# Performance work log

Hardware: AMD Instinct MI355X
Metric: run time of the kernel (lower is better)

## Reference

```python
import jax, jax.numpy as jnp
import numpy as np

IB = 8; WB = 8; ABMVM = 8; ABNM = 8; N_MSB = 4; NL = 0.0  # noise_level=0 -> deterministic
B = 4096; IN = 1024; H = 1024

sg = jax.lax.stop_gradient

def quant_raw(x, bits, r):
    step = 2.0 ** (bits - 1)
    xs = jnp.clip(x / r, -1.0 + 1.0 / step, 1.0 - 1.0 / step)
    return jnp.round(xs * step) / step * r

def quant_ste(x, bits, r):
    # straight-through: value = quantized, grad = identity wrt x, no grad to r
    return x + sg(quant_raw(x, bits, r) - x)

def pact(x, a):
    # sign(x)*0.5*(|x| - ||x|-a| + a) == clamp(x, -a, a), kept literal for fidelity
    return jnp.sign(x) * 0.5 * (jnp.abs(x) - jnp.abs(jnp.abs(x) - a) + a)

def bitsplit(x, bits, n_msb):
    # symmetric bit-splitting; STE backward: each y_i has identity grad wrt x
    ste = x - sg(x)
    xv = sg(x)
    beta = 1.0
    ys = []
    for _ in range(n_msb):
        y = quant_raw(xv / beta, bits, 1.0)
        xv = xv - y * beta
        ys.append(y + ste)
        beta = beta / 2.0
    betas = jnp.asarray([1.0 / (2.0 ** i) for i in range(n_msb)], dtype=x.dtype)
    return jnp.stack(ys), betas  # [n_msb, B, D], [n_msb]

def custom_mm(inp, w, b, key):
    # forward: inp @ (quant(clamp(w)) + noise) + quant(b) + noise
    # backward (torch custom): grads use RAW w/b -> STE via out_lin path
    kw, kb = jax.random.split(key)
    n = inp.shape[0]
    noise_w = jax.random.normal(kw, (n, w.shape[1], w.shape[2]), dtype=w.dtype) * NL
    noise_b = jax.random.normal(kb, (n, 1, b.shape[2]), dtype=b.dtype) * NL
    wq = quant_raw(jnp.clip(w, -1.0, 1.0), WB, 1.0)
    bq = quant_raw(b, WB, 1.0)
    out_val = jnp.einsum('nbi,nio->nbo', inp, wq + noise_w) + (bq + noise_b)
    out_lin = jnp.einsum('nbi,io->nbo', inp, w[0]) + b
    return out_lin + sg(out_val - out_lin)

def _cell(input, hx, cx, weight_ih, weight_hh, bias_ih, bias_hh,
          a1, a3, a4, a5, a6, a7, a8, a9, a10, a11):
    k1, k2 = jax.random.split(jax.random.key(42))
    ys, betas = bitsplit(pact(input, a1) / a1, IB, N_MSB)
    out_q = quant_ste(custom_mm(ys, weight_ih, bias_ih, k1), ABMVM, 1.0)
    part1 = (betas[:, None, None] * out_q).sum(0) * a1          # [B, 4H]
    ys, betas = bitsplit(pact(hx, a11) / a11, IB, N_MSB)
    out_q = quant_ste(custom_mm(ys, weight_hh, bias_hh, k2), ABMVM, 1.0)
    part2 = (betas[:, None, None] * out_q).sum(0) * a11
    gates = part1 + part2
    i, j, f, o = jnp.split(gates, 4, axis=1)
    fg = quant_ste(pact(jax.nn.sigmoid(f), a3), ABNM, a3)
    ig = quant_ste(pact(jax.nn.sigmoid(i), a4), ABNM, a4)
    act = quant_ste(pact(jnp.tanh(j), a5), ABNM, a5)
    og = quant_ste(pact(jax.nn.sigmoid(o), a6), ABNM, a6)
    gc = quant_ste(pact(cx * fg, a7), ABNM, a7)
    ai = quant_ste(pact(ig * act, a8), ABNM, a8)
    new_c = quant_ste(pact(gc + ai, a9), ABNM, a9)
    ac = quant_ste(pact(jnp.tanh(new_c), a10), ABNM, a10)
    new_h = quant_ste(pact(ac * og, a11), ABNM, a11)
    return jnp.stack([new_h, new_c])  # [2, B, H]

def setup_inputs() -> dict:
    key = jax.random.key(0)
    ks = jax.random.split(key, 7)
    return {
        'input': jax.random.normal(ks[0], (B, IN), dtype=jnp.float32),
        'hx': jax.random.normal(ks[1], (B, H), dtype=jnp.float32),
        'cx': jax.random.normal(ks[2], (B, H), dtype=jnp.float32),
        'weight_ih': jax.random.normal(ks[3], (1, IN, 4 * H), dtype=jnp.float32) * 0.05,
        'weight_hh': jax.random.normal(ks[4], (1, H, 4 * H), dtype=jnp.float32) * 0.05,
        'bias_ih': jax.random.normal(ks[5], (1, 1, 4 * H), dtype=jnp.float32) * 0.05,
        'bias_hh': jax.random.normal(ks[6], (1, 1, 4 * H), dtype=jnp.float32) * 0.05,
        'a1': jnp.array([128.0]), 'a3': jnp.array([1.0]), 'a4': jnp.array([1.0]),
        'a5': jnp.array([1.0]), 'a6': jnp.array([1.0]), 'a7': jnp.array([4.0]),
        'a8': jnp.array([1.0]), 'a9': jnp.array([4.0]), 'a10': jnp.array([1.0]),
        'a11': jnp.array([4.0]),
    }

def reference(input, hx, cx, weight_ih, weight_hh, bias_ih, bias_hh,
              a1, a3, a4, a5, a6, a7, a8, a9, a10, a11):
    return _cell(input, hx, cx, weight_ih, weight_hh, bias_ih, bias_hh,
                 a1, a3, a4, a5, a6, a7, a8, a9, a10, a11)
```

## Files before the change

### kernel.cpp

```cpp
#include <hip/hip_runtime.h>
#include <cstdint>

typedef unsigned short u16;
typedef __attribute__((ext_vector_type(4))) int i32x4;

#define DEVI __device__ __forceinline__

DEVI float pactf(float x, float a) {
    float ax = fabsf(x);
    float w  = fabsf(ax - a);
    float t  = (ax - w) + a;
    float s  = (x > 0.f) ? 0.5f : ((x < 0.f) ? -0.5f : 0.0f);
    return s * t;
}
DEVI float quantf(float x, float r) {
    float xs = x / r;
    xs = fminf(fmaxf(xs, -0.9921875f), 0.9921875f);
    float e = rintf(xs * 128.0f);
    return (e * 0.0078125f) * r;
}
DEVI float sigf(float x) {
    float eg  = (float)exp(-(double)x);
    float den = 1.0f + eg;
    return 1.0f / den;
}
DEVI float tanf32(float x) { return (float)tanh((double)x); }

#define KSIG  4436
#define NSIG  8873
#define KTANH 2309
#define NTANH 4619

__global__ void prep_tables(float* __restrict__ Ts, float* __restrict__ Tt) {
    int i = blockIdx.x * 256 + threadIdx.x;
    if (i < NSIG)  Ts[i] = sigf((float)(i - KSIG)  * 0.00390625f);
    if (i < NTANH) Tt[i] = tanf32((float)(i - KTANH) * 0.00390625f);
}

DEVI float sig_lut(float g, const float* __restrict__ Ts) {
    float g256 = g * 256.0f;
    float kf = rintf(g256);
    if (kf == g256) {
        if (kf >  (float)KSIG) return 1.0f;
        if (kf < -(float)KSIG) return 0.0f;
        return Ts[(int)kf + KSIG];
    }
    return sigf(g);
}
DEVI float tanh_lut(float g, const float* __restrict__ Tt) {
    float g256 = g * 256.0f;
    float kf = rintf(g256);
    if (kf == g256) {
        if (fabsf(kf) <= (float)KTANH) return Tt[(int)kf + KTANH];
        return copysignf(1.0f, g);
    }
    return tanf32(g);
}

__global__ void prep_act_f(const float* __restrict__ X, const float* __restrict__ ap,
                           signed char* __restrict__ A, int planebase) {
    int idx4 = (blockIdx.x * 256 + threadIdx.x) * 4;
    float a = ap[0];
    float4 xv4 = *(const float4*)(X + idx4);
    float v[4] = {xv4.x, xv4.y, xv4.z, xv4.w};
    signed char e4[4][4];
#pragma unroll
    for (int el = 0; el < 4; el++) {
        float x = pactf(v[el], a) / a;
        float xv = x;
        float beta = 1.0f;
#pragma unroll
        for (int n = 0; n < 4; n++) {
            float xs = xv / beta;
            xs = fminf(fmaxf(xs, -0.9921875f), 0.9921875f);
            float e = rintf(xs * 128.0f);
            e4[n][el] = (signed char)(int)e;
            float y = e * 0.0078125f;
            xv = xv - y * beta;
            beta = beta * 0.5f;
        }
    }
#pragma unroll
    for (int n = 0; n < 4; n++)
        *(char4*)(A + (size_t)(planebase + n) * 4194304u + idx4) =
            make_char4(e4[n][0], e4[n][1], e4[n][2], e4[n][3]);
}

__global__ void prep_w(const float* __restrict__ W0, const float* __restrict__ W1,
                       signed char* __restrict__ Wt) {
    __shared__ float tile[32][33];
    int proj = blockIdx.z;
    const float* W = proj ? W1 : W0;
    int n0 = blockIdx.x * 32, k0 = blockIdx.y * 32;
    int tx = threadIdx.x, ty = threadIdx.y;
#pragma unroll
    for (int i = 0; i < 4; i++)
        tile[ty + i * 8][tx] = W[(size_t)(k0 + ty + i * 8) * 4096 + n0 + tx];
    __syncthreads();
#pragma unroll
    for (int i = 0; i < 4; i++) {
        float w = tile[tx][ty + i * 8];
        float xs = fminf(fmaxf(w, -0.9921875f), 0.9921875f);
        float e = rintf(xs * 128.f);
        Wt[(size_t)proj * 4194304u + (size_t)(n0 + ty + i * 8) * 1024 + k0 + tx] =
            (signed char)(int)e;
    }
}

__global__ void prep_bias(const float* __restrict__ b0, const float* __restrict__ b1,
                          float* __restrict__ Bf) {
    int idx = blockIdx.x * 256 + threadIdx.x;
    const float* b = (idx < 4096) ? b0 : b1;
    float v = b[idx & 4095];
    float xs = fminf(fmaxf(v, -0.9921875f), 0.9921875f);
    Bf[idx] = rintf(xs * 128.f);
}

#define GLOAD16(gp, lp) __builtin_amdgcn_global_load_lds( \
    (const __attribute__((address_space(1))) void*)(gp),  \
    (__attribute__((address_space(3))) void*)(lp), 16, 0, 0)

__global__ __launch_bounds__(256) void gemm_planes(
    const signed char* __restrict__ A, const signed char* __restrict__ Wt,
    const float* __restrict__ Bf, signed char* __restrict__ E) {
    __shared__ __align__(16) signed char lds[16384];
    int tid = threadIdx.x;
    int c0 = blockIdx.x * 128;
    int r0 = blockIdx.y * 128;
    int proj = (r0 >= 16384) ? 1 : 0;

    const signed char* gA = A + (size_t)(r0 + (tid >> 2)) * 1024 + (tid & 3) * 16;
    const signed char* gB = Wt + (size_t)proj * 4194304u + (size_t)(c0 + (tid >> 2)) * 1024 + (tid & 3) * 16;

    signed char* lA0 = lds + tid * 16;
    signed char* lA1 = lds + 4096 + tid * 16;
    signed char* lB0 = lds + 8192 + tid * 16;
    signed char* lB1 = lds + 12288 + tid * 16;

    int w = tid >> 6, l = tid & 63;
    int wm = (w >> 1) * 64, wn = (w & 1) * 64;
    int quad = l >> 4, lrow = l & 15;

    const signed char* fA = lds + (wm + lrow) * 64 + quad * 16;
    const signed char* fB = lds + 8192 + (wn + lrow) * 64 + quad * 16;

    i32x4 acc[4][4] = {};

    for (int k0 = 0; k0 < 1024; k0 += 64) {
        GLOAD16(gA, lA0);
        GLOAD16(gA + 64 * 1024, lA1);
        GLOAD16(gB, lB0);
        GLOAD16(gB + 64 * 1024, lB1);
        gA += 64; gB += 64;
        asm volatile("s_waitcnt vmcnt(0)" ::: "memory");
        __syncthreads();
        i32x4 af[4], bfr[4];
#pragma unroll
        for (int mt = 0; mt < 4; mt++) af[mt] = *(const i32x4*)(fA + mt * 1024);
#pragma unroll
        for (int nt = 0; nt < 4; nt++) bfr[nt] = *(const i32x4*)(fB + nt * 1024);
#pragma unroll
        for (int mt = 0; mt < 4; mt++)
#pragma unroll
            for (int nt = 0; nt < 4; nt++)
                acc[mt][nt] = __builtin_amdgcn_mfma_i32_16x16x64_i8(
                    af[mt], bfr[nt], acc[mt][nt], 0, 0, 0);
        __syncthreads();
    }

    signed char* ctile = lds;
#pragma unroll
    for (int nt = 0; nt < 4; nt++) {
        int lc = wn + nt * 16 + lrow;
        float bb = Bf[proj * 4096 + c0 + lc];
#pragma unroll
        for (int mt = 0; mt < 4; mt++) {
            int lr = wm + mt * 16 + quad * 4;
#pragma unroll
            for (int r = 0; r < 4; r++) {
                float t = (float)acc[mt][nt][r] * 0.0078125f + bb;
                float tc = fminf(fmaxf(t, -127.f), 127.f);
                ctile[(lr + r) * 128 + lc] = (signed char)(int)rintf(tc);
            }
        }
    }
    __syncthreads();
#pragma unroll
    for (int p = 0; p < 4; p++) {
        int lr = (tid >> 3) + p * 32;
        int lc = (tid & 7) * 16;
        *(int4*)(E + (size_t)(r0 + lr) * 4096 + c0 + lc) =
            *(const int4*)(ctile + lr * 128 + lc);
    }
}

__global__ __launch_bounds__(256) void gates_kernel_t(
    const signed char* __restrict__ E, const float* __restrict__ cx,
    float* __restrict__ out,
    const float* __restrict__ TsG, const float* __restrict__ TtG,
    const float* __restrict__ a1p, const float* __restrict__ a3p,
    const float* __restrict__ a4p, const float* __restrict__ a5p,
    const float* __restrict__ a6p, const float* __restrict__ a7p,
    const float* __restrict__ a8p, const float* __restrict__ a9p,
    const float* __restrict__ a10p, const float* __restrict__ a11p) {
    __shared__ float Ts[NSIG];
    __shared__ float Tt[NTANH];
    int tid = threadIdx.x;
    for (int i = tid; i < NSIG; i += 256) Ts[i] = TsG[i];
    for (int i = tid; i < NTANH; i += 256) Tt[i] = TtG[i];
    __syncthreads();

    int b = blockIdx.x;
    int h0 = tid * 4;
    float a1 = a1p[0], a3 = a3p[0], a4 = a4p[0], a5 = a5p[0], a6 = a6p[0];
    float a7 = a7p[0], a8 = a8p[0], a9 = a9p[0], a10 = a10p[0], a11 = a11p[0];

    float gate[4][4];
#pragma unroll
    for (int g = 0; g < 4; g++) {
        size_t colbase = (size_t)g * 1024 + h0;
        int s1[4] = {0, 0, 0, 0}, s2[4] = {0, 0, 0, 0};
#pragma unroll
        for (int n = 0; n < 4; n++) {
            char4 e1 = *(const char4*)(E + (((size_t)(n * 4096 + b)) << 12) + colbase);
            char4 e2 = *(const char4*)(E + (((size_t)((4 + n) * 4096 + b)) << 12) + colbase);
            int wgt = 8 >> n;
            s1[0] += (int)e1.x * wgt; s1[1] += (int)e1.y * wgt;
            s1[2] += (int)e1.z * wgt; s1[3] += (int)e1.w * wgt;
            s2[0] += (int)e2.x * wgt; s2[1] += (int)e2.y * wgt;
            s2[2] += (int)e2.z * wgt; s2[3] += (int)e2.w * wgt;
        }
#pragma unroll
        for (int jj = 0; jj < 4; jj++) {
            float p1 = ((float)s1[jj] * 0.0009765625f) * a1;
            float p2 = ((float)s2[jj] * 0.0009765625f) * a11;
            gate[g][jj] = p1 + p2;
        }
    }

    float4 cxv = *(const float4*)(cx + (size_t)b * 1024 + h0);
    float cxa[4] = {cxv.x, cxv.y, cxv.z, cxv.w};
    float nh[4], ncv[4];
#pragma unroll
    for (int jj = 0; jj < 4; jj++) {
        float gi = gate[0][jj], gj = gate[1][jj], gf = gate[2][jj], go = gate[3][jj];
        float fg  = quantf(pactf(sig_lut(gf, Ts), a3), a3);
        float ig  = quantf(pactf(sig_lut(gi, Ts), a4), a4);
        float act = quantf(pactf(tanh_lut(gj, Tt), a5), a5);
        float og  = quantf(pactf(sig_lut(go, Ts), a6), a6);
        float gc  = quantf(pactf(cxa[jj] * fg, a7), a7);
        float ai  = quantf(pactf(ig * act, a8), a8);
        float nc  = quantf(pactf(gc + ai, a9), a9);
        float ac  = quantf(pactf(tanh_lut(nc, Tt), a10), a10);
        float hh  = quantf(pactf(ac * og, a11), a11);
        nh[jj]  = hh;
        ncv[jj] = nc;
    }
    float4 o1 = {nh[0], nh[1], nh[2], nh[3]};
    float4 o2 = {ncv[0], ncv[1], ncv[2], ncv[3]};
    *(float4*)(out + (size_t)b * 1024 + h0) = o1;
    *(float4*)(out + 4194304u + (size_t)b * 1024 + h0) = o2;
}

extern "C" void kernel_launch(void* const* d_in, const int* in_sizes, int n_in,
                              void* d_out, int out_size, void* d_ws, size_t ws_size,
                              hipStream_t stream) {
    const float* input = (const float*)d_in[0];
    const float* hx    = (const float*)d_in[1];
    const float* cx    = (const float*)d_in[2];
    const float* wih   = (const float*)d_in[3];
    const float* whh   = (const float*)d_in[4];
    const float* bih   = (const float*)d_in[5];
    const float* bhh   = (const float*)d_in[6];
    const float* a1  = (const float*)d_in[7];
    const float* a3  = (const float*)d_in[8];
    const float* a4  = (const float*)d_in[9];
    const float* a5  = (const float*)d_in[10];
    const float* a6  = (const float*)d_in[11];
    const float* a7  = (const float*)d_in[12];
    const float* a8  = (const float*)d_in[13];
    const float* a9  = (const float*)d_in[14];
    const float* a10 = (const float*)d_in[15];
    const float* a11 = (const float*)d_in[16];

    char* ws = (char*)d_ws;
    signed char* A  = (signed char*)ws;
    signed char* Wt = (signed char*)(ws + 33554432);
    float*       Bf = (float*)(ws + 41943040);
    float*       Ts = (float*)(ws + 41975808);
    float*       Tt = (float*)(ws + 42011300);
    signed char* E  = (signed char*)(ws + 42041344);

    prep_tables<<<35, 256, 0, stream>>>(Ts, Tt);
    prep_act_f<<<4096, 256, 0, stream>>>(input, a1, A, 0);
    prep_act_f<<<4096, 256, 0, stream>>>(hx, a11, A, 4);
    prep_w<<<dim3(128, 32, 2), dim3(32, 8), 0, stream>>>(wih, whh, Wt);
    prep_bias<<<32, 256, 0, stream>>>(bih, bhh, Bf);
    gemm_planes<<<dim3(32, 256), 256, 0, stream>>>(A, Wt, Bf, E);
    gates_kernel_t<<<4096, 256, 0, stream>>>(E, cx, (float*)d_out, Ts, Tt,
                                             a1, a3, a4, a5, a6, a7, a8, a9, a10, a11);
}
```

Before: 380.1 us.

## Double-buffer GEMM LDS tiles, merge prep kernels, read LUTs from global

The int8 plane GEMM now uses two LDS buffers, so the next K-slice is loaded by global_load_lds while MFMAs run on the current one. This removes the per-iteration full vmcnt(0) stall, at the cost of doubling LDS per block, which may lower occupancy. The table and bias prep kernels are merged, and the two activation-prep launches become one, cutting launch count. The gates kernel stops copying the sigmoid/tanh tables into shared memory and reads them from global memory, which avoids about 54KB of LDS fill per block but makes the lookups go through the cache.

```diff
diff --git a/kernel.cpp b/kernel.cpp
--- a/kernel.cpp
+++ b/kernel.cpp
@@ -30,12 +30,6 @@
 #define NSIG  8873
 #define KTANH 2309
 #define NTANH 4619
-
-__global__ void prep_tables(float* __restrict__ Ts, float* __restrict__ Tt) {
-    int i = blockIdx.x * 256 + threadIdx.x;
-    if (i < NSIG)  Ts[i] = sigf((float)(i - KSIG)  * 0.00390625f);
-    if (i < NTANH) Tt[i] = tanf32((float)(i - KTANH) * 0.00390625f);
-}
 
 DEVI float sig_lut(float g, const float* __restrict__ Ts) {
     float g256 = g * 256.0f;
@@ -57,10 +51,29 @@
     return tanf32(g);
 }
 
-__global__ void prep_act_f(const float* __restrict__ X, const float* __restrict__ ap,
-                           signed char* __restrict__ A, int planebase) {
-    int idx4 = (blockIdx.x * 256 + threadIdx.x) * 4;
-    float a = ap[0];
+__global__ void prep_misc(const float* __restrict__ b0, const float* __restrict__ b1,
+                          float* __restrict__ Bf, float* __restrict__ Ts,
+                          float* __restrict__ Tt) {
+    int i = blockIdx.x * 256 + threadIdx.x;
+    if (i < NSIG)  Ts[i] = sigf((float)(i - KSIG)  * 0.00390625f);
+    if (i < NTANH) Tt[i] = tanf32((float)(i - KTANH) * 0.00390625f);
+    if (i < 8192) {
+        const float* b = (i < 4096) ? b0 : b1;
+        float v = b[i & 4095];
+        float xs = fminf(fmaxf(v, -0.9921875f), 0.9921875f);
+        Bf[i] = rintf(xs * 128.f);
+    }
+}
+
+__global__ void prep_act2(const float* __restrict__ X0, const float* __restrict__ X1,
+                          const float* __restrict__ a1p, const float* __restrict__ a11p,
+                          signed char* __restrict__ A) {
+    int blk = blockIdx.x;
+    int lo = (blk < 4096) ? 1 : 0;
+    const float* X = lo ? X0 : X1;
+    float a = lo ? a1p[0] : a11p[0];
+    int planebase = lo ? 0 : 4;
+    int idx4 = ((blk & 4095) * 256 + threadIdx.x) * 4;
     float4 xv4 = *(const float4*)(X + idx4);
     float v[4] = {xv4.x, xv4.y, xv4.z, xv4.w};
     signed char e4[4][4];
@@ -107,15 +120,6 @@
     }
 }
 
-__global__ void prep_bias(const float* __restrict__ b0, const float* __restrict__ b1,
-                          float* __restrict__ Bf) {
-    int idx = blockIdx.x * 256 + threadIdx.x;
-    const float* b = (idx < 4096) ? b0 : b1;
-    float v = b[idx & 4095];
-    float xs = fminf(fmaxf(v, -0.9921875f), 0.9921875f);
-    Bf[idx] = rintf(xs * 128.f);
-}
-
 #define GLOAD16(gp, lp) __builtin_amdgcn_global_load_lds( \
     (const __attribute__((address_space(1))) void*)(gp),  \
     (__attribute__((address_space(3))) void*)(lp), 16, 0, 0)
@@ -123,7 +127,7 @@
 __global__ __launch_bounds__(256) void gemm_planes(
     const signed char* __restrict__ A, const signed char* __restrict__ Wt,
     const float* __restrict__ Bf, signed char* __restrict__ E) {
-    __shared__ __align__(16) signed char lds[16384];
+    __shared__ __align__(16) signed char lds[32768];
     int tid = threadIdx.x;
     int c0 = blockIdx.x * 128;
     int r0 = blockIdx.y * 128;
@@ -132,41 +136,57 @@
     const signed char* gA = A + (size_t)(r0 + (tid >> 2)) * 1024 + (tid & 3) * 16;
     const signed char* gB = Wt + (size_t)proj * 4194304u + (size_t)(c0 + (tid >> 2)) * 1024 + (tid & 3) * 16;
 
-    signed char* lA0 = lds + tid * 16;
-    signed char* lA1 = lds + 4096 + tid * 16;
-    signed char* lB0 = lds + 8192 + tid * 16;
-    signed char* lB1 = lds + 12288 + tid * 16;
-
     int w = tid >> 6, l = tid & 63;
     int wm = (w >> 1) * 64, wn = (w & 1) * 64;
     int quad = l >> 4, lrow = l & 15;
 
-    const signed char* fA = lds + (wm + lrow) * 64 + quad * 16;
-    const signed char* fB = lds + 8192 + (wn + lrow) * 64 + quad * 16;
+    int stoff = tid * 16;
+    int fAoff = (wm + lrow) * 64 + quad * 16;
+    int fBoff = 8192 + (wn + lrow) * 64 + quad * 16;
 
     i32x4 acc[4][4] = {};
 
-    for (int k0 = 0; k0 < 1024; k0 += 64) {
-        GLOAD16(gA, lA0);
-        GLOAD16(gA + 64 * 1024, lA1);
-        GLOAD16(gB, lB0);
-        GLOAD16(gB + 64 * 1024, lB1);
-        gA += 64; gB += 64;
-        asm volatile("s_waitcnt vmcnt(0)" ::: "memory");
+#define STAGE(bufbase)                                        \
+    do {                                                      \
+        signed char* lb = lds + (bufbase) + stoff;            \
+        GLOAD16(gA,             lb);                          \
+        GLOAD16(gA + 64 * 1024, lb + 4096);                   \
+        GLOAD16(gB,             lb + 8192);                   \
+        GLOAD16(gB + 64 * 1024, lb + 12288);                  \
+        gA += 64; gB += 64;                                   \
+    } while (0)
+
+#define COMPUTE(bufbase)                                      \
+    do {                                                      \
+        const signed char* fA = lds + (bufbase) + fAoff;      \
+        const signed char* fB = lds + (bufbase) + fBoff;      \
+        i32x4 af[4], bfr[4];                                  \
+        _Pragma("unroll")                                     \
+        for (int mt = 0; mt < 4; mt++) af[mt] = *(const i32x4*)(fA + mt * 1024);  \
+        _Pragma("unroll")                                     \
+        for (int nt = 0; nt < 4; nt++) bfr[nt] = *(const i32x4*)(fB + nt * 1024); \
+        _Pragma("unroll")                                     \
+        for (int mt = 0; mt < 4; mt++)                        \
+            _Pragma("unroll")                                 \
+            for (int nt = 0; nt < 4; nt++)                    \
+                acc[mt][nt] = __builtin_amdgcn_mfma_i32_16x16x64_i8( \
+                    af[mt], bfr[nt], acc[mt][nt], 0, 0, 0);   \
+    } while (0)
+
+    STAGE(0);
+    asm volatile("s_waitcnt vmcnt(0)" ::: "memory");
+    __syncthreads();
+
+    for (int k0 = 0; k0 < 1024; k0 += 128) {
+        STAGE(16384);
+        COMPUTE(0);
         __syncthreads();
-        i32x4 af[4], bfr[4];
-#pragma unroll
-        for (int mt = 0; mt < 4; mt++) af[mt] = *(const i32x4*)(fA + mt * 1024);
-#pragma unroll
-        for (int nt = 0; nt < 4; nt++) bfr[nt] = *(const i32x4*)(fB + nt * 1024);
-#pragma unroll
-        for (int mt = 0; mt < 4; mt++)
-#pragma unroll
-            for (int nt = 0; nt < 4; nt++)
-                acc[mt][nt] = __builtin_amdgcn_mfma_i32_16x16x64_i8(
-                    af[mt], bfr[nt], acc[mt][nt], 0, 0, 0);
+        if (k0 + 128 < 1024) STAGE(0);
+        COMPUTE(16384);
         __syncthreads();
     }
+#undef STAGE
+#undef COMPUTE
 
     signed char* ctile = lds;
 #pragma unroll
@@ -197,19 +217,13 @@
 __global__ __launch_bounds__(256) void gates_kernel_t(
     const signed char* __restrict__ E, const float* __restrict__ cx,
     float* __restrict__ out,
-    const float* __restrict__ TsG, const float* __restrict__ TtG,
+    const float* __restrict__ Ts, const float* __restrict__ Tt,
     const float* __restrict__ a1p, const float* __restrict__ a3p,
     const float* __restrict__ a4p, const float* __restrict__ a5p,
     const float* __restrict__ a6p, const float* __restrict__ a7p,
     const float* __restrict__ a8p, const float* __restrict__ a9p,
     const float* __restrict__ a10p, const float* __restrict__ a11p) {
-    __shared__ float Ts[NSIG];
-    __shared__ float Tt[NTANH];
     int tid = threadIdx.x;
-    for (int i = tid; i < NSIG; i += 256) Ts[i] = TsG[i];
-    for (int i = tid; i < NTANH; i += 256) Tt[i] = TtG[i];
-    __syncthreads();
-
     int b = blockIdx.x;
     int h0 = tid * 4;
     float a1 = a1p[0], a3 = a3p[0], a4 = a4p[0], a5 = a5p[0], a6 = a6p[0];
@@ -291,11 +305,9 @@
     float*       Tt = (float*)(ws + 42011300);
     signed char* E  = (signed char*)(ws + 42041344);
 
-    prep_tables<<<35, 256, 0, stream>>>(Ts, Tt);
-    prep_act_f<<<4096, 256, 0, stream>>>(input, a1, A, 0);
-    prep_act_f<<<4096, 256, 0, stream>>>(hx, a11, A, 4);
+    prep_misc<<<35, 256, 0, stream>>>(bih, bhh, Bf, Ts, Tt);
+    prep_act2<<<8192, 256, 0, stream>>>(input, hx, a1, a11, A);
     prep_w<<<dim3(128, 32, 2), dim3(32, 8), 0, stream>>>(wih, whh, Wt);
-    prep_bias<<<32, 256, 0, stream>>>(bih, bhh, Bf);
     gemm_planes<<<dim3(32, 256), 256, 0, stream>>>(A, Wt, Bf, E);
     gates_kernel_t<<<4096, 256, 0, stream>>>(E, cx, (float*)d_out, Ts, Tt,
                                              a1, a3, a4, a5, a6, a7, a8, a9, a10, a11);
```

New measurement: 374.3 us. About the same (-1.5%).
